# Kernel tuning notes

Measured on AMD Instinct MI355X. Metric: run time of the kernel, lower is better.

Reference implementation:

```python
import jax, jax.numpy as jnp
import numpy as np
import math

B, S, D, H = 1, 4096, 1024, 16
HD = D // H  # head_dim = 64


def setup_inputs() -> dict:
    key = jax.random.key(0)
    ks = jax.random.split(key, 6)
    x = jax.random.normal(ks[0], (B, S, D), dtype=jnp.float32)
    # Llama-style rotary frequencies: theta = 10000^{-2i/head_dim}
    inv_freq = 1.0 / (10000.0 ** (jnp.arange(0, HD, 2, dtype=jnp.float32) / HD))  # (HD/2,)
    t = jnp.arange(S, dtype=jnp.float32)
    freqs = jnp.outer(t, inv_freq)  # (S, HD/2)
    cos = jnp.cos(freqs)
    sin = jnp.sin(freqs)
    # additive causal mask (S, S): 0 on/below diagonal, -inf above
    mask = jnp.where(jnp.tril(jnp.ones((S, S), dtype=bool)), 0.0, -jnp.inf).astype(jnp.float32)
    scale = 1.0 / math.sqrt(D)
    wq = jax.random.normal(ks[1], (D, D), dtype=jnp.float32) * scale
    wk = jax.random.normal(ks[2], (D, D), dtype=jnp.float32) * scale
    wv = jax.random.normal(ks[3], (D, D), dtype=jnp.float32) * scale
    wo = jax.random.normal(ks[4], (D, D), dtype=jnp.float32) * scale
    return {"x": x, "cos": cos, "sin": sin, "mask": mask,
            "wq": wq, "wk": wk, "wv": wv, "wo": wo, "start_pos": 0}


def _rope(t, cos, sin):
    # t: (b, s, h, hd); cos/sin: (s, hd/2). Interleaved-pair complex rotation.
    b, s, h, hd = t.shape
    tr = t.reshape(b, s, h, hd // 2, 2)
    te, to = tr[..., 0], tr[..., 1]
    c = cos[None, :, None, :]
    sn = sin[None, :, None, :]
    oe = te * c - to * sn
    oo = te * sn + to * c
    return jnp.stack([oe, oo], axis=-1).reshape(b, s, h, hd)


def reference(x, cos, sin, mask, wq, wk, wv, wo, start_pos):
    b, s, d = x.shape
    h, hd = H, HD
    # Linear layers: y = x @ W.T (torch nn.Linear convention, W is (out,in))
    xq = (x @ wq.T).reshape(b, s, h, hd)
    xk = (x @ wk.T).reshape(b, s, h, hd)
    xv = (x @ wv.T).reshape(b, s, h, hd)
    xq = _rope(xq, cos, sin)
    xk = _rope(xk, cos, sin)
    # (b, h, s, hd)
    xq = xq.transpose(0, 2, 1, 3)
    xk = xk.transpose(0, 2, 1, 3)
    xv = xv.transpose(0, 2, 1, 3)
    scores = jnp.einsum('bhqd,bhkd->bhqk', xq, xk) / math.sqrt(hd)
    scores = scores + mask[None, None, :, :]
    attn = jax.nn.softmax(scores.astype(jnp.float32), axis=-1).astype(xq.dtype)
    out = jnp.einsum('bhqk,bhkd->bhqd', attn, xv)
    out = out.transpose(0, 2, 1, 3).reshape(b, s, d)
    return out @ wo.T
```

## Files before the change

### kernel.cpp

```cpp
#include <hip/hip_runtime.h>
#include <hip/hip_bf16.h>
#include <math.h>

typedef __bf16 bf16;
typedef __bf16 bf16x4 __attribute__((ext_vector_type(4)));
typedef __bf16 bf16x8 __attribute__((ext_vector_type(8)));
typedef float floatx4 __attribute__((ext_vector_type(4)));
typedef short short4v __attribute__((ext_vector_type(4)));

#define S_LEN 4096
#define DM 1024
#define NH 16
#define HD 64

#define GM 4096
#define GN 1024
#define GK 1024

#define GLDS16(gp, lp) __builtin_amdgcn_global_load_lds( \
    (const __attribute__((address_space(1))) void*)(gp), \
    (__attribute__((address_space(3))) void*)(lp), 16, 0, 0)

__global__ void cvt_bf16(const float* __restrict__ x,  const float* __restrict__ wq,
                         const float* __restrict__ wk, const float* __restrict__ wv,
                         const float* __restrict__ wo, bf16* __restrict__ dst)
{
    size_t i4 = ((size_t)blockIdx.x * 256 + threadIdx.x) * 4;
    const float* src; size_t off;
    const size_t M1 = (size_t)1 << 20;
    if      (i4 < 4 * M1) { src = x;  off = i4;          }
    else if (i4 < 5 * M1) { src = wq; off = i4 - 4 * M1; }
    else if (i4 < 6 * M1) { src = wk; off = i4 - 5 * M1; }
    else if (i4 < 7 * M1) { src = wv; off = i4 - 6 * M1; }
    else                  { src = wo; off = i4 - 7 * M1; }
    float4 v = *(const float4*)(src + off);
    bf16x4 o = { (bf16)v.x, (bf16)v.y, (bf16)v.z, (bf16)v.w };
    *(bf16x4*)(&dst[i4]) = o;
}

__launch_bounds__(256)
__global__ void gemm_qkv(const bf16* __restrict__ A,
                         const bf16* __restrict__ B0, const bf16* __restrict__ B1,
                         const bf16* __restrict__ B2,
                         const float* __restrict__ cosp, const float* __restrict__ sinp,
                         bf16* __restrict__ Qw, bf16* __restrict__ Kw,
                         bf16* __restrict__ VTw)
{
    const int bz = blockIdx.z;
    const bf16* __restrict__ B = (bz == 0) ? B0 : (bz == 1 ? B1 : B2);

    const int tid  = threadIdx.x;
    const int wave = tid >> 6;
    const int lane = tid & 63;
    const int wm   = (wave >> 1) * 32;
    const int wn   = (wave & 1) * 64;
    const int lrow = lane >> 4;
    const int lcol = lane & 15;

    const int m0 = blockIdx.y * 64;
    const int n0 = blockIdx.x * 128;

    __shared__ __align__(16) bf16 As[64 * 64];
    __shared__ __align__(16) bf16 Bs[128 * 64];

    floatx4 acc[2][4];
    #pragma unroll
    for (int i = 0; i < 2; i++)
        #pragma unroll
        for (int j = 0; j < 4; j++) acc[i][j] = (floatx4){0.f, 0.f, 0.f, 0.f};

    const bf16* ga0 = A + (size_t)(m0 + wave * 16 + (lane >> 3)) * GK + (lane & 7) * 8;
    const bf16* gb0 = B + (size_t)(n0 + wave * 32 + (lane >> 3)) * GK + (lane & 7) * 8;
    bf16* la = &As[(wave * 16) * 64];
    bf16* lb = &Bs[(wave * 32) * 64];

    for (int kt = 0; kt < GK; kt += 64) {
        #pragma unroll
        for (int i = 0; i < 2; i++)
            GLDS16(ga0 + kt + (size_t)i * 8 * GK, la + i * 8 * 64);
        #pragma unroll
        for (int i = 0; i < 4; i++)
            GLDS16(gb0 + kt + (size_t)i * 8 * GK, lb + i * 8 * 64);
        __syncthreads();
        #pragma unroll
        for (int ks = 0; ks < 2; ks++) {
            bf16x8 af[2], bfr[4];
            #pragma unroll
            for (int t = 0; t < 2; t++)
                af[t]  = *(const bf16x8*)(&As[(wm + t * 16 + lcol) * 64 + ks * 32 + lrow * 8]);
            #pragma unroll
            for (int t = 0; t < 4; t++)
                bfr[t] = *(const bf16x8*)(&Bs[(wn + t * 16 + lcol) * 64 + ks * 32 + lrow * 8]);
            #pragma unroll
            for (int mt = 0; mt < 2; mt++)
                #pragma unroll
                for (int nt = 0; nt < 4; nt++)
                    acc[mt][nt] = __builtin_amdgcn_mfma_f32_16x16x32_bf16(af[mt], bfr[nt], acc[mt][nt], 0, 0, 0);
        }
        __syncthreads();
    }

    if (bz < 2) {
        bf16* __restrict__ C = bz ? Kw : Qw;
        const bool odd = (lcol & 1);
        #pragma unroll
        for (int mt = 0; mt < 2; mt++)
            #pragma unroll
            for (int nt = 0; nt < 4; nt++) {
                int i = (nt * 16 + lcol) >> 1;
                #pragma unroll
                for (int r = 0; r < 4; r++) {
                    float v  = acc[mt][nt][r];
                    float pv = __shfl_xor(v, 1, 64);
                    int s = m0 + wm + mt * 16 + lrow * 4 + r;
                    float c  = cosp[s * 32 + i];
                    float sn = sinp[s * 32 + i];
                    float ov = odd ? (pv * sn + v * c) : (v * c - pv * sn);
                    C[(size_t)s * GN + n0 + wn + nt * 16 + lcol] = (bf16)ov;
                }
            }
    } else {
        #pragma unroll
        for (int mt = 0; mt < 2; mt++)
            #pragma unroll
            for (int nt = 0; nt < 4; nt++) {
                int col = n0 + wn + nt * 16 + lcol;
                int s   = m0 + wm + mt * 16 + lrow * 4;
                bf16x4 ov = { (bf16)acc[mt][nt][0], (bf16)acc[mt][nt][1],
                              (bf16)acc[mt][nt][2], (bf16)acc[mt][nt][3] };
                *(bf16x4*)(&VTw[(size_t)col * S_LEN + s]) = ov;
            }
    }
}

#define KSW(row, chunk) (((row) << 6) + ((((chunk) ^ ((row) & 7))) << 3))

template<int STEP>
__launch_bounds__(256, 4)
__global__ void flash_attn(const bf16* __restrict__ Q, const bf16* __restrict__ K,
                           const bf16* __restrict__ VT,
                           float* __restrict__ O0, float* __restrict__ O1,
                           float* __restrict__ O2,
                           float* __restrict__ L0, float* __restrict__ L1,
                           float* __restrict__ L2)
{
    const int pi   = blockIdx.x / STEP;
    const int p    = blockIdx.x % STEP;
    const int h    = blockIdx.y;
    const int tid  = threadIdx.x;
    const int wave = tid >> 6;
    const int lane = tid & 63;
    const int lrow = lane >> 4;
    const int lcol = lane & 15;
    const int rsw  = lcol & 7;

    const int qtA = pi;
    const int qtB = 63 - pi;

    float* __restrict__ Op = (p == 0) ? O0 : (p == 1 ? O1 : O2);
    float* __restrict__ Lp = (p == 0) ? L0 : (p == 1 ? L1 : L2);

    __shared__ __align__(16) bf16 Ks[2][64 * 64];
    __shared__ __align__(16) bf16 Vs[2][64 * 64];

    const float sc2 = 0.125f * 1.44269504088896340736f;

    const int q0A = qtA * 64 + wave * 16;
    const int q0B = qtB * 64 + wave * 16;

    const bf16* qpA = Q + (size_t)(q0A + lcol) * DM + h * HD;
    const bf16* qpB = Q + (size_t)(q0B + lcol) * DM + h * HD;
    bf16x8 qfA[2], qfB[2];
    qfA[0] = *(const bf16x8*)(qpA + 0 + lrow * 8);
    qfA[1] = *(const bf16x8*)(qpA + 32 + lrow * 8);
    qfB[0] = *(const bf16x8*)(qpB + 0 + lrow * 8);
    qfB[1] = *(const bf16x8*)(qpB + 32 + lrow * 8);

    floatx4 lA4 = (floatx4){0.f, 0.f, 0.f, 0.f};
    floatx4 lB4 = (floatx4){0.f, 0.f, 0.f, 0.f};
    floatx4 oaccA[4], oaccB[4];
    #pragma unroll
    for (int nt = 0; nt < 4; nt++) {
        oaccA[nt] = (floatx4){0.f, 0.f, 0.f, 0.f};
        oaccB[nt] = (floatx4){0.f, 0.f, 0.f, 0.f};
    }

    const int  srow = tid >> 3;
    const int  schk = tid & 7;
    const bf16* kp  = K  + (size_t)srow * DM + h * HD + schk * 8;
    const bf16* vp  = VT + (size_t)(h * HD + srow) * S_LEN + schk * 8;
    const int  wof  = KSW(srow, schk);

    {
        size_t ko = (size_t)p * 64 * DM;
        size_t vo = (size_t)p * 64;
        uint4 a = *(const uint4*)(kp + ko);
        uint4 b = *(const uint4*)(kp + ko + (size_t)32 * DM);
        uint4 c = *(const uint4*)(vp + vo);
        uint4 d = *(const uint4*)(vp + vo + (size_t)32 * S_LEN);
        *(uint4*)(&Ks[0][wof])           = a;
        *(uint4*)(&Ks[0][wof + 32 * 64]) = b;
        *(uint4*)(&Vs[0][wof])           = c;
        *(uint4*)(&Vs[0][wof + 32 * 64]) = d;
    }
    __syncthreads();

    uint4 kr0, kr1, vr0, vr1;
    for (int t = p; t <= qtB; t += STEP) {
        const int  cur  = ((t - p) / STEP) & 1;
        const bool more = (t + STEP <= qtB);
        const bool actA = (t <= qtA);

        if (more) {
            size_t ko = (size_t)(t + STEP) * 64 * DM;
            size_t vo = (size_t)(t + STEP) * 64;
            kr0 = *(const uint4*)(kp + ko);
            kr1 = *(const uint4*)(kp + ko + (size_t)32 * DM);
            vr0 = *(const uint4*)(vp + vo);
            vr1 = *(const uint4*)(vp + vo + (size_t)32 * S_LEN);
        }

        short4v pbA[4], pbB[4];
        const bool diagA = (t == qtA);
        const bool diagB = (t == qtB);
        #pragma unroll
        for (int nt = 0; nt < 4; nt++) {
            floatx4 zB = (floatx4){0.f, 0.f, 0.f, 0.f};
            floatx4 zA = (floatx4){0.f, 0.f, 0.f, 0.f};
            __builtin_amdgcn_s_setprio(1);
            #pragma unroll
            for (int ks = 0; ks < 2; ks++) {
                bf16x8 kf = *(const bf16x8*)(&Ks[cur][((nt * 16 + lcol) << 6) +
                                             ((((ks << 2) + lrow) ^ rsw) << 3)]);
                zB = __builtin_amdgcn_mfma_f32_16x16x32_bf16(kf, qfB[ks], zB, 0, 0, 0);
                if (actA)
                    zA = __builtin_amdgcn_mfma_f32_16x16x32_bf16(kf, qfA[ks], zA, 0, 0, 0);
            }
            __builtin_amdgcn_s_setprio(0);
            if (diagB) {
                #pragma unroll
                for (int r = 0; r < 4; r++) {
                    int kg = t * 64 + nt * 16 + lrow * 4 + r;
                    float pr = exp2f(zB[r] * sc2);
                    if (kg > q0B + lcol) pr = 0.f;
                    zB[r] = pr; lB4[r] += pr;
                }
            } else {
                #pragma unroll
                for (int r = 0; r < 4; r++) {
                    float pr = exp2f(zB[r] * sc2);
                    zB[r] = pr; lB4[r] += pr;
                }
            }
            bf16x4 pvB = { (bf16)zB[0], (bf16)zB[1], (bf16)zB[2], (bf16)zB[3] };
            pbB[nt] = __builtin_bit_cast(short4v, pvB);
            if (actA) {
                if (diagA) {
                    #pragma unroll
                    for (int r = 0; r < 4; r++) {
                        int kg = t * 64 + nt * 16 + lrow * 4 + r;
                        float pr = exp2f(zA[r] * sc2);
                        if (kg > q0A + lcol) pr = 0.f;
                        zA[r] = pr; lA4[r] += pr;
                    }
                } else {
                    #pragma unroll
                    for (int r = 0; r < 4; r++) {
                        float pr = exp2f(zA[r] * sc2);
                        zA[r] = pr; lA4[r] += pr;
                    }
                }
                bf16x4 pvA = { (bf16)zA[0], (bf16)zA[1], (bf16)zA[2], (bf16)zA[3] };
                pbA[nt] = __builtin_bit_cast(short4v, pvA);
            }
        }

        __builtin_amdgcn_s_setprio(1);
        #pragma unroll
        for (int nt = 0; nt < 4; nt++)
            #pragma unroll
            for (int kt = 0; kt < 4; kt++) {
                bf16x4 va = *(const bf16x4*)(&Vs[cur][((nt * 16 + lcol) << 6) +
                              ((((kt << 1) + (lrow >> 1)) ^ rsw) << 3) + ((lrow & 1) << 2)]);
                short4v vas = __builtin_bit_cast(short4v, va);
                oaccB[nt] = __builtin_amdgcn_mfma_f32_16x16x16bf16_1k(vas, pbB[kt], oaccB[nt], 0, 0, 0);
                if (actA)
                    oaccA[nt] = __builtin_amdgcn_mfma_f32_16x16x16bf16_1k(vas, pbA[kt], oaccA[nt], 0, 0, 0);
            }
        __builtin_amdgcn_s_setprio(0);

        if (more) {
            int nxt = cur ^ 1;
            *(uint4*)(&Ks[nxt][wof])           = kr0;
            *(uint4*)(&Ks[nxt][wof + 32 * 64]) = kr1;
            *(uint4*)(&Vs[nxt][wof])           = vr0;
            *(uint4*)(&Vs[nxt][wof + 32 * 64]) = vr1;
        }
        __syncthreads();
    }

    float lA = lA4[0] + lA4[1] + lA4[2] + lA4[3];
    float lB = lB4[0] + lB4[1] + lB4[2] + lB4[3];
    lA += __shfl_xor(lA, 16, 64);
    lA += __shfl_xor(lA, 32, 64);
    lB += __shfl_xor(lB, 16, 64);
    lB += __shfl_xor(lB, 32, 64);
    if (lrow == 0) {
        Lp[h * S_LEN + q0A + lcol] = lA;
        Lp[h * S_LEN + q0B + lcol] = lB;
    }
    #pragma unroll
    for (int nt = 0; nt < 4; nt++) {
        *(floatx4*)(&Op[(size_t)(q0A + lcol) * DM + h * HD + nt * 16 + lrow * 4]) = oaccA[nt];
        *(floatx4*)(&Op[(size_t)(q0B + lcol) * DM + h * HD + nt * 16 + lrow * 4]) = oaccB[nt];
    }
}

__global__ void combine2(const float* __restrict__ O0, const float* __restrict__ O1,
                         const float* __restrict__ L0, const float* __restrict__ L1,
                         bf16* __restrict__ Aw)
{
    int i4 = (blockIdx.x * 256 + threadIdx.x) * 4;
    int q = i4 >> 10;
    int c = i4 & 1023;
    int h = c >> 6;
    float rl = 1.f / (L0[h * S_LEN + q] + L1[h * S_LEN + q]);
    float4 a = *(const float4*)(O0 + i4);
    float4 b = *(const float4*)(O1 + i4);
    bf16x4 o = { (bf16)((a.x + b.x) * rl), (bf16)((a.y + b.y) * rl),
                 (bf16)((a.z + b.z) * rl), (bf16)((a.w + b.w) * rl) };
    *(bf16x4*)(&Aw[i4]) = o;
}

__global__ void combine3(const float* __restrict__ O0, const float* __restrict__ O1,
                         const float* __restrict__ O2,
                         const float* __restrict__ L0, const float* __restrict__ L1,
                         const float* __restrict__ L2,
                         bf16* __restrict__ Aw)
{
    int i4 = (blockIdx.x * 256 + threadIdx.x) * 4;
    int q = i4 >> 10;
    int c = i4 & 1023;
    int h = c >> 6;
    float rl = 1.f / (L0[h * S_LEN + q] + L1[h * S_LEN + q] + L2[h * S_LEN + q]);
    float4 a = *(const float4*)(O0 + i4);
    float4 b = *(const float4*)(O1 + i4);
    float4 cc = *(const float4*)(O2 + i4);
    bf16x4 o = { (bf16)((a.x + b.x + cc.x) * rl), (bf16)((a.y + b.y + cc.y) * rl),
                 (bf16)((a.z + b.z + cc.z) * rl), (bf16)((a.w + b.w + cc.w) * rl) };
    *(bf16x4*)(&Aw[i4]) = o;
}

__launch_bounds__(256)
__global__ void gemm_out(const bf16* __restrict__ A, const bf16* __restrict__ B,
                         float* __restrict__ out)
{
    const int tid  = threadIdx.x;
    const int wave = tid >> 6;
    const int lane = tid & 63;
    const int wm   = (wave >> 1) * 32;
    const int wn   = (wave & 1) * 64;
    const int lrow = lane >> 4;
    const int lcol = lane & 15;

    const int m0 = blockIdx.y * 64;
    const int n0 = blockIdx.x * 128;

    __shared__ __align__(16) bf16 As[64 * 64];
    __shared__ __align__(16) bf16 Bs[128 * 64];

    floatx4 acc[2][4];
    #pragma unroll
    for (int i = 0; i < 2; i++)
        #pragma unroll
        for (int j = 0; j < 4; j++) acc[i][j] = (floatx4){0.f, 0.f, 0.f, 0.f};

    const bf16* ga0 = A + (size_t)(m0 + wave * 16 + (lane >> 3)) * GK + (lane & 7) * 8;
    const bf16* gb0 = B + (size_t)(n0 + wave * 32 + (lane >> 3)) * GK + (lane & 7) * 8;
    bf16* la = &As[(wave * 16) * 64];
    bf16* lb = &Bs[(wave * 32) * 64];

    for (int kt = 0; kt < GK; kt += 64) {
        #pragma unroll
        for (int i = 0; i < 2; i++)
            GLDS16(ga0 + kt + (size_t)i * 8 * GK, la + i * 8 * 64);
        #pragma unroll
        for (int i = 0; i < 4; i++)
            GLDS16(gb0 + kt + (size_t)i * 8 * GK, lb + i * 8 * 64);
        __syncthreads();
        #pragma unroll
        for (int ks = 0; ks < 2; ks++) {
            bf16x8 af[2], bfr[4];
            #pragma unroll
            for (int t = 0; t < 2; t++)
                af[t]  = *(const bf16x8*)(&As[(wm + t * 16 + lcol) * 64 + ks * 32 + lrow * 8]);
            #pragma unroll
            for (int t = 0; t < 4; t++)
                bfr[t] = *(const bf16x8*)(&Bs[(wn + t * 16 + lcol) * 64 + ks * 32 + lrow * 8]);
            #pragma unroll
            for (int mt = 0; mt < 2; mt++)
                #pragma unroll
                for (int nt = 0; nt < 4; nt++)
                    acc[mt][nt] = __builtin_amdgcn_mfma_f32_16x16x32_bf16(af[mt], bfr[nt], acc[mt][nt], 0, 0, 0);
        }
        __syncthreads();
    }

    #pragma unroll
    for (int mt = 0; mt < 2; mt++)
        #pragma unroll
        for (int nt = 0; nt < 4; nt++)
            #pragma unroll
            for (int r = 0; r < 4; r++) {
                int row = m0 + wm + mt * 16 + lrow * 4 + r;
                int col = n0 + wn + nt * 16 + lcol;
                out[(size_t)row * GN + col] = acc[mt][nt][r];
            }
}

extern "C" void kernel_launch(void* const* d_in, const int* in_sizes, int n_in,
                              void* d_out, int out_size, void* d_ws, size_t ws_size,
                              hipStream_t stream) {
    const float* x    = (const float*)d_in[0];
    const float* cosp = (const float*)d_in[1];
    const float* sinp = (const float*)d_in[2];
    const float* wq   = (const float*)d_in[4];
    const float* wk   = (const float*)d_in[5];
    const float* wv   = (const float*)d_in[6];
    const float* wo   = (const float*)d_in[7];
    float* out = (float*)d_out;

    const size_t SD = (size_t)S_LEN * DM;
    const size_t DD = (size_t)DM * DM;
    bf16* xb  = (bf16*)d_ws;
    bf16* wqb = xb + SD;
    bf16* wkb = wqb + DD;
    bf16* wvb = wkb + DD;
    bf16* wob = wvb + DD;
    bf16* Qw  = wob + DD;
    bf16* Kw  = Qw + SD;
    bf16* VTw = Kw + SD;
    bf16* Aw  = VTw + SD;
    float* O0f = (float*)(Aw + SD);
    float* O1f = O0f + SD;
    float* L0f = O1f + SD;
    float* L1f = L0f + (size_t)S_LEN * NH;
    float* O2f = L1f + (size_t)S_LEN * NH;
    float* L2f = O2f + SD;
    size_t need3 = (size_t)((char*)(L2f + (size_t)S_LEN * NH) - (char*)d_ws);

    cvt_bf16<<<8192, 256, 0, stream>>>(x, wq, wk, wv, wo, xb);
    gemm_qkv<<<dim3(GN / 128, GM / 64, 3), 256, 0, stream>>>(
        xb, wqb, wkb, wvb, cosp, sinp, Qw, Kw, VTw);
    if (ws_size >= need3) {
        flash_attn<3><<<dim3(96, NH), 256, 0, stream>>>(
            Qw, Kw, VTw, O0f, O1f, O2f, L0f, L1f, L2f);
        combine3<<<S_LEN * DM / 1024, 256, 0, stream>>>(
            O0f, O1f, O2f, L0f, L1f, L2f, Aw);
    } else {
        flash_attn<2><<<dim3(64, NH), 256, 0, stream>>>(
            Qw, Kw, VTw, O0f, O1f, O0f, L0f, L1f, L0f);
        combine2<<<S_LEN * DM / 1024, 256, 0, stream>>>(
            O0f, O1f, L0f, L1f, Aw);
    }
    gemm_out<<<dim3(GN / 128, GM / 64), 256, 0, stream>>>(Aw, wob, out);
}
```

Before: 305.6 us.

## Enlarge GEMM tiles to 128x128 and drop three-way attention split

The QKV and output projection GEMMs now use 128x128 block tiles, with each wave computing a 64x64 subtile. This doubles MFMA work per LDS load and halves global-to-LDS traffic per output. The three-way key-split attention path and its combine kernel are removed, so attention always uses the two-way split. Risks are fewer blocks for the GEMMs (lower occupancy and tail fill on 256 CUs), higher register pressure, and less attention parallelism if the three-way path was previously taken.

```diff
diff --git a/kernel.cpp b/kernel.cpp
--- a/kernel.cpp
+++ b/kernel.cpp
@@ -52,47 +52,46 @@
     const int tid  = threadIdx.x;
     const int wave = tid >> 6;
     const int lane = tid & 63;
-    const int wm   = (wave >> 1) * 32;
+    const int wm   = (wave >> 1) * 64;
     const int wn   = (wave & 1) * 64;
     const int lrow = lane >> 4;
     const int lcol = lane & 15;
 
-    const int m0 = blockIdx.y * 64;
+    const int m0 = blockIdx.y * 128;
     const int n0 = blockIdx.x * 128;
 
-    __shared__ __align__(16) bf16 As[64 * 64];
+    __shared__ __align__(16) bf16 As[128 * 64];
     __shared__ __align__(16) bf16 Bs[128 * 64];
 
-    floatx4 acc[2][4];
+    floatx4 acc[4][4];
     #pragma unroll
-    for (int i = 0; i < 2; i++)
+    for (int i = 0; i < 4; i++)
         #pragma unroll
         for (int j = 0; j < 4; j++) acc[i][j] = (floatx4){0.f, 0.f, 0.f, 0.f};
 
-    const bf16* ga0 = A + (size_t)(m0 + wave * 16 + (lane >> 3)) * GK + (lane & 7) * 8;
-    const bf16* gb0 = B + (size_t)(n0 + wave * 32 + (lane >> 3)) * GK + (lane & 7) * 8;
-    bf16* la = &As[(wave * 16) * 64];
-    bf16* lb = &Bs[(wave * 32) * 64];
+    const bf16* ga0 = A + (size_t)(m0 + wave * 8 + (lane >> 3)) * GK + (lane & 7) * 8;
+    const bf16* gb0 = B + (size_t)(n0 + wave * 8 + (lane >> 3)) * GK + (lane & 7) * 8;
+    bf16* la = &As[(wave * 8) * 64];
+    bf16* lb = &Bs[(wave * 8) * 64];
 
     for (int kt = 0; kt < GK; kt += 64) {
         #pragma unroll
-        for (int i = 0; i < 2; i++)
-            GLDS16(ga0 + kt + (size_t)i * 8 * GK, la + i * 8 * 64);
-        #pragma unroll
-        for (int i = 0; i < 4; i++)
-            GLDS16(gb0 + kt + (size_t)i * 8 * GK, lb + i * 8 * 64);
+        for (int i = 0; i < 4; i++) {
+            GLDS16(ga0 + kt + (size_t)(i * 32) * GK, la + i * 32 * 64);
+            GLDS16(gb0 + kt + (size_t)(i * 32) * GK, lb + i * 32 * 64);
+        }
         __syncthreads();
         #pragma unroll
         for (int ks = 0; ks < 2; ks++) {
-            bf16x8 af[2], bfr[4];
-            #pragma unroll
-            for (int t = 0; t < 2; t++)
+            bf16x8 af[4], bfr[4];
+            #pragma unroll
+            for (int t = 0; t < 4; t++)
                 af[t]  = *(const bf16x8*)(&As[(wm + t * 16 + lcol) * 64 + ks * 32 + lrow * 8]);
             #pragma unroll
             for (int t = 0; t < 4; t++)
                 bfr[t] = *(const bf16x8*)(&Bs[(wn + t * 16 + lcol) * 64 + ks * 32 + lrow * 8]);
             #pragma unroll
-            for (int mt = 0; mt < 2; mt++)
+            for (int mt = 0; mt < 4; mt++)
                 #pragma unroll
                 for (int nt = 0; nt < 4; nt++)
                     acc[mt][nt] = __builtin_amdgcn_mfma_f32_16x16x32_bf16(af[mt], bfr[nt], acc[mt][nt], 0, 0, 0);
@@ -104,7 +103,7 @@
         bf16* __restrict__ C = bz ? Kw : Qw;
         const bool odd = (lcol & 1);
         #pragma unroll
-        for (int mt = 0; mt < 2; mt++)
+        for (int mt = 0; mt < 4; mt++)
             #pragma unroll
             for (int nt = 0; nt < 4; nt++) {
                 int i = (nt * 16 + lcol) >> 1;
@@ -121,7 +120,7 @@
             }
     } else {
         #pragma unroll
-        for (int mt = 0; mt < 2; mt++)
+        for (int mt = 0; mt < 4; mt++)
             #pragma unroll
             for (int nt = 0; nt < 4; nt++) {
                 int col = n0 + wn + nt * 16 + lcol;
@@ -140,9 +139,7 @@
 __global__ void flash_attn(const bf16* __restrict__ Q, const bf16* __restrict__ K,
                            const bf16* __restrict__ VT,
                            float* __restrict__ O0, float* __restrict__ O1,
-                           float* __restrict__ O2,
-                           float* __restrict__ L0, float* __restrict__ L1,
-                           float* __restrict__ L2)
+                           float* __restrict__ L0, float* __restrict__ L1)
 {
     const int pi   = blockIdx.x / STEP;
     const int p    = blockIdx.x % STEP;
@@ -157,8 +154,8 @@
     const int qtA = pi;
     const int qtB = 63 - pi;
 
-    float* __restrict__ Op = (p == 0) ? O0 : (p == 1 ? O1 : O2);
-    float* __restrict__ Lp = (p == 0) ? L0 : (p == 1 ? L1 : L2);
+    float* __restrict__ Op = p ? O1 : O0;
+    float* __restrict__ Lp = p ? L1 : L0;
 
     __shared__ __align__(16) bf16 Ks[2][64 * 64];
     __shared__ __align__(16) bf16 Vs[2][64 * 64];
@@ -332,25 +329,6 @@
     *(bf16x4*)(&Aw[i4]) = o;
 }
 
-__global__ void combine3(const float* __restrict__ O0, const float* __restrict__ O1,
-                         const float* __restrict__ O2,
-                         const float* __restrict__ L0, const float* __restrict__ L1,
-                         const float* __restrict__ L2,
-                         bf16* __restrict__ Aw)
-{
-    int i4 = (blockIdx.x * 256 + threadIdx.x) * 4;
-    int q = i4 >> 10;
-    int c = i4 & 1023;
-    int h = c >> 6;
-    float rl = 1.f / (L0[h * S_LEN + q] + L1[h * S_LEN + q] + L2[h * S_LEN + q]);
-    float4 a = *(const float4*)(O0 + i4);
-    float4 b = *(const float4*)(O1 + i4);
-    float4 cc = *(const float4*)(O2 + i4);
-    bf16x4 o = { (bf16)((a.x + b.x + cc.x) * rl), (bf16)((a.y + b.y + cc.y) * rl),
-                 (bf16)((a.z + b.z + cc.z) * rl), (bf16)((a.w + b.w + cc.w) * rl) };
-    *(bf16x4*)(&Aw[i4]) = o;
-}
-
 __launch_bounds__(256)
 __global__ void gemm_out(const bf16* __restrict__ A, const bf16* __restrict__ B,
                          float* __restrict__ out)
@@ -358,47 +336,46 @@
     const int tid  = threadIdx.x;
     const int wave = tid >> 6;
     const int lane = tid & 63;
-    const int wm   = (wave >> 1) * 32;
+    const int wm   = (wave >> 1) * 64;
     const int wn   = (wave & 1) * 64;
     const int lrow = lane >> 4;
     const int lcol = lane & 15;
 
-    const int m0 = blockIdx.y * 64;
+    const int m0 = blockIdx.y * 128;
     const int n0 = blockIdx.x * 128;
 
-    __shared__ __align__(16) bf16 As[64 * 64];
+    __shared__ __align__(16) bf16 As[128 * 64];
     __shared__ __align__(16) bf16 Bs[128 * 64];
 
-    floatx4 acc[2][4];
+    floatx4 acc[4][4];
     #pragma unroll
-    for (int i = 0; i < 2; i++)
+    for (int i = 0; i < 4; i++)
         #pragma unroll
         for (int j = 0; j < 4; j++) acc[i][j] = (floatx4){0.f, 0.f, 0.f, 0.f};
 
-    const bf16* ga0 = A + (size_t)(m0 + wave * 16 + (lane >> 3)) * GK + (lane & 7) * 8;
-    const bf16* gb0 = B + (size_t)(n0 + wave * 32 + (lane >> 3)) * GK + (lane & 7) * 8;
-    bf16* la = &As[(wave * 16) * 64];
-    bf16* lb = &Bs[(wave * 32) * 64];
+    const bf16* ga0 = A + (size_t)(m0 + wave * 8 + (lane >> 3)) * GK + (lane & 7) * 8;
+    const bf16* gb0 = B + (size_t)(n0 + wave * 8 + (lane >> 3)) * GK + (lane & 7) * 8;
+    bf16* la = &As[(wave * 8) * 64];
+    bf16* lb = &Bs[(wave * 8) * 64];
 
     for (int kt = 0; kt < GK; kt += 64) {
         #pragma unroll
-        for (int i = 0; i < 2; i++)
-            GLDS16(ga0 + kt + (size_t)i * 8 * GK, la + i * 8 * 64);
-        #pragma unroll
-        for (int i = 0; i < 4; i++)
-            GLDS16(gb0 + kt + (size_t)i * 8 * GK, lb + i * 8 * 64);
+        for (int i = 0; i < 4; i++) {
+            GLDS16(ga0 + kt + (size_t)(i * 32) * GK, la + i * 32 * 64);
+            GLDS16(gb0 + kt + (size_t)(i * 32) * GK, lb + i * 32 * 64);
+        }
         __syncthreads();
         #pragma unroll
         for (int ks = 0; ks < 2; ks++) {
-            bf16x8 af[2], bfr[4];
-            #pragma unroll
-            for (int t = 0; t < 2; t++)
+            bf16x8 af[4], bfr[4];
+            #pragma unroll
+            for (int t = 0; t < 4; t++)
                 af[t]  = *(const bf16x8*)(&As[(wm + t * 16 + lcol) * 64 + ks * 32 + lrow * 8]);
             #pragma unroll
             for (int t = 0; t < 4; t++)
                 bfr[t] = *(const bf16x8*)(&Bs[(wn + t * 16 + lcol) * 64 + ks * 32 + lrow * 8]);
             #pragma unroll
-            for (int mt = 0; mt < 2; mt++)
+            for (int mt = 0; mt < 4; mt++)
                 #pragma unroll
                 for (int nt = 0; nt < 4; nt++)
                     acc[mt][nt] = __builtin_amdgcn_mfma_f32_16x16x32_bf16(af[mt], bfr[nt], acc[mt][nt], 0, 0, 0);
@@ -407,7 +384,7 @@
     }
 
     #pragma unroll
-    for (int mt = 0; mt < 2; mt++)
+    for (int mt = 0; mt < 4; mt++)
         #pragma unroll
         for (int nt = 0; nt < 4; nt++)
             #pragma unroll
@@ -445,23 +422,12 @@
     float* O1f = O0f + SD;
     float* L0f = O1f + SD;
     float* L1f = L0f + (size_t)S_LEN * NH;
-    float* O2f = L1f + (size_t)S_LEN * NH;
-    float* L2f = O2f + SD;
-    size_t need3 = (size_t)((char*)(L2f + (size_t)S_LEN * NH) - (char*)d_ws);
 
     cvt_bf16<<<8192, 256, 0, stream>>>(x, wq, wk, wv, wo, xb);
-    gemm_qkv<<<dim3(GN / 128, GM / 64, 3), 256, 0, stream>>>(
+    gemm_qkv<<<dim3(GN / 128, GM / 128, 3), 256, 0, stream>>>(
         xb, wqb, wkb, wvb, cosp, sinp, Qw, Kw, VTw);
-    if (ws_size >= need3) {
-        flash_attn<3><<<dim3(96, NH), 256, 0, stream>>>(
-            Qw, Kw, VTw, O0f, O1f, O2f, L0f, L1f, L2f);
-        combine3<<<S_LEN * DM / 1024, 256, 0, stream>>>(
-            O0f, O1f, O2f, L0f, L1f, L2f, Aw);
-    } else {
-        flash_attn<2><<<dim3(64, NH), 256, 0, stream>>>(
-            Qw, Kw, VTw, O0f, O1f, O0f, L0f, L1f, L0f);
-        combine2<<<S_LEN * DM / 1024, 256, 0, stream>>>(
-            O0f, O1f, L0f, L1f, Aw);
-    }
-    gemm_out<<<dim3(GN / 128, GM / 64), 256, 0, stream>>>(Aw, wob, out);
-}
+    flash_attn<2><<<dim3(64, NH), 256, 0, stream>>>(
+        Qw, Kw, VTw, O0f, O1f, L0f, L1f);
+    combine2<<<S_LEN * DM / 1024, 256, 0, stream>>>(O0f, O1f, L0f, L1f, Aw);
+    gemm_out<<<dim3(GN / 128, GM / 128), 256, 0, stream>>>(Aw, wob, out);
+}
```

New measurement: 317.7 us. 3.9% more time.
